# Performance work log

Measured on AMD Instinct MI355X. Metric: run time of the kernel, lower is better.

The kernel has to match this reference:

```python
import jax, jax.numpy as jnp
import numpy as np

B, LP, LR = 16, 128, 1024
D = 128
DG = 640  # 5 * 128 concat
K = 7     # number of FC trans heads
EDGE_P = 0.05


def _gcn_block(x, adj, mask, W1, b1, W2, b2):
    # x: [B,L,DG], adj: [B,L,L] (nonzero => edge weight 1, like dense_to_sparse + GCNConv)
    A = (adj != 0).astype(x.dtype)
    L = A.shape[-1]
    eye = jnp.eye(L, dtype=x.dtype)
    Ah = jnp.maximum(A, eye)                     # add_remaining_self_loops
    deg = Ah.sum(axis=1)                         # col degree [B,L] (gcn_norm uses target index)
    dinv = jax.lax.rsqrt(deg)                    # deg >= 1 thanks to self loops
    N = Ah * dinv[:, :, None] * dinv[:, None, :] # normalized adjacency per edge (r,c)
    agg = lambda h: jnp.einsum('brc,brd->bcd', N, h)  # aggregate sources r into target c
    h1 = jax.nn.relu(agg(x @ W1) + b1)
    h2 = agg(h1 @ W2) + b2
    return jax.nn.relu(x + h2) * mask[..., None]


def _fc_trans(feature, Wt, bt):
    # feature: [B,L,DG]; Wt: [K,D,DG]; bt: [K,D]
    h = jnp.einsum('bld,kod->kblo', feature, Wt) + bt[:, None, None, :]
    h = jax.nn.relu(h)                 # FCNet [640->128], ReLU (dropout off in eval)
    return jnp.swapaxes(h, 2, 3)       # [K,B,D,L] (transpose(1,2))


def _forward(x_pep, x_ss_pep, x_2_pep, x_dense_pep, x_pretrain_pep,
             x_pro, x_ss_pro, x_2_pro, x_dense_pro, x_pretrain_pro,
             x_edge_pep, x_edge_pro, x_seqmask_pep, x_seqmask_pro,
             E_seq, E_ss, E_two, W_dpep, b_dpep, W_dpro, b_dpro,
             W_ppep, b_ppep, W_ppro, b_ppro,
             Wg_pep1, bg_pep1, Wg_pep2, bg_pep2,
             Wg_pro1, bg_pro1, Wg_pro2, bg_pro2,
             Wt_pep, bt_pep, Wt_pro, bt_pro):
    enc_pep = jnp.concatenate([
        E_seq[x_pep], E_ss[x_ss_pep], E_two[x_2_pep],
        x_dense_pep @ W_dpep + b_dpep,
        x_pretrain_pep @ W_ppep + b_ppep], axis=-1) * x_seqmask_pep[..., None]
    enc_pro = jnp.concatenate([
        E_seq[x_pro], E_ss[x_ss_pro], E_two[x_2_pro],
        x_dense_pro @ W_dpro + b_dpro,
        x_pretrain_pro @ W_ppro + b_ppro], axis=-1) * x_seqmask_pro[..., None]

    f_pep = _gcn_block(enc_pep, x_edge_pep, x_seqmask_pep, Wg_pep1, bg_pep1, Wg_pep2, bg_pep2)
    f_pro = _gcn_block(enc_pro, x_edge_pro, x_seqmask_pro, Wg_pro1, bg_pro1, Wg_pro2, bg_pro2)

    pep_vecs = _fc_trans(f_pep, Wt_pep, bt_pep)[..., None]        # [K,B,D,LP,1] (unsqueeze 3)
    pro_vecs = _fc_trans(f_pro, Wt_pro, bt_pro)[:, :, :, None, :]  # [K,B,D,1,LR] (unsqueeze 2)
    return pep_vecs, pro_vecs


def setup_inputs() -> dict:
    key = jax.random.key(0)
    ks = jax.random.split(key, 40)
    f32 = jnp.float32
    s = 0.05
    inp = {
        'x_pep': jax.random.randint(ks[0], (B, LP), 0, 25),
        'x_ss_pep': jax.random.randint(ks[1], (B, LP), 0, 73),
        'x_2_pep': jax.random.randint(ks[2], (B, LP), 0, 8),
        'x_dense_pep': jax.random.normal(ks[3], (B, LP, 3), f32),
        'x_pretrain_pep': jax.random.normal(ks[4], (B, LP, 1024), f32),
        'x_pro': jax.random.randint(ks[5], (B, LR), 0, 25),
        'x_ss_pro': jax.random.randint(ks[6], (B, LR), 0, 73),
        'x_2_pro': jax.random.randint(ks[7], (B, LR), 0, 8),
        'x_dense_pro': jax.random.normal(ks[8], (B, LR, 23), f32),
        'x_pretrain_pro': jax.random.normal(ks[9], (B, LR, 1024), f32),
        'x_edge_pep': (jax.random.uniform(ks[10], (B, LP, LP)) < EDGE_P).astype(f32),
        'x_edge_pro': (jax.random.uniform(ks[11], (B, LR, LR)) < EDGE_P).astype(f32),
        'x_seqmask_pep': jnp.ones((B, LP), f32),
        'x_seqmask_pro': jnp.ones((B, LR), f32),
        'E_seq': jax.random.normal(ks[12], (25, D), f32) * s,
        'E_ss': jax.random.normal(ks[13], (73, D), f32) * s,
        'E_two': jax.random.normal(ks[14], (8, D), f32) * s,
        'W_dpep': jax.random.normal(ks[15], (3, D), f32) * s,
        'b_dpep': jnp.zeros((D,), f32),
        'W_dpro': jax.random.normal(ks[16], (23, D), f32) * s,
        'b_dpro': jnp.zeros((D,), f32),
        'W_ppep': jax.random.normal(ks[17], (1024, D), f32) * s,
        'b_ppep': jnp.zeros((D,), f32),
        'W_ppro': jax.random.normal(ks[18], (1024, D), f32) * s,
        'b_ppro': jnp.zeros((D,), f32),
        'Wg_pep1': jax.random.normal(ks[19], (DG, DG), f32) * s,
        'bg_pep1': jnp.zeros((DG,), f32),
        'Wg_pep2': jax.random.normal(ks[20], (DG, DG), f32) * s,
        'bg_pep2': jnp.zeros((DG,), f32),
        'Wg_pro1': jax.random.normal(ks[21], (DG, DG), f32) * s,
        'bg_pro1': jnp.zeros((DG,), f32),
        'Wg_pro2': jax.random.normal(ks[22], (DG, DG), f32) * s,
        'bg_pro2': jnp.zeros((DG,), f32),
        'Wt_pep': jax.random.normal(ks[23], (K, D, DG), f32) * s,
        'bt_pep': jnp.zeros((K, D), f32),
        'Wt_pro': jax.random.normal(ks[24], (K, D, DG), f32) * s,
        'bt_pro': jnp.zeros((K, D), f32),
    }
    return inp


def reference(x_pep, x_ss_pep, x_2_pep, x_dense_pep, x_pretrain_pep,
              x_pro, x_ss_pro, x_2_pro, x_dense_pro, x_pretrain_pro,
              x_edge_pep, x_edge_pro, x_seqmask_pep, x_seqmask_pro,
              E_seq, E_ss, E_two, W_dpep, b_dpep, W_dpro, b_dpro,
              W_ppep, b_ppep, W_ppro, b_ppro,
              Wg_pep1, bg_pep1, Wg_pep2, bg_pep2,
              Wg_pro1, bg_pro1, Wg_pro2, bg_pro2,
              Wt_pep, bt_pep, Wt_pro, bt_pro):
    return _forward(x_pep, x_ss_pep, x_2_pep, x_dense_pep, x_pretrain_pep,
                    x_pro, x_ss_pro, x_2_pro, x_dense_pro, x_pretrain_pro,
                    x_edge_pep, x_edge_pro, x_seqmask_pep, x_seqmask_pro,
                    E_seq, E_ss, E_two, W_dpep, b_dpep, W_dpro, b_dpro,
                    W_ppep, b_ppep, W_ppro, b_ppro,
                    Wg_pep1, bg_pep1, Wg_pep2, bg_pep2,
                    Wg_pro1, bg_pro1, Wg_pro2, bg_pro2,
                    Wt_pep, bt_pep, Wt_pro, bt_pro)
```

## Files before the change

### kernel.cpp

```cpp
#include <hip/hip_runtime.h>
#include <hip/hip_bf16.h>

#define BSZ 16
#define LP 128
#define LR 1024
#define DD 128
#define DG 640
#define KH 7
#define SPLITK 4

typedef __bf16 bf16x8 __attribute__((ext_vector_type(8)));
typedef __bf16 bf16x4v __attribute__((ext_vector_type(4)));
typedef float f32x4 __attribute__((ext_vector_type(4)));
typedef unsigned int uint32;

__device__ __forceinline__ void gl16(const void* g, void* l) {
  __builtin_amdgcn_global_load_lds(
      (const __attribute__((address_space(1))) unsigned int*)g,
      (__attribute__((address_space(3))) unsigned int*)l, 16, 0, 0);
}

__device__ __forceinline__ void mfma_core_lds(
    const ushort* __restrict__ Ab, int lda,
    const ushort* __restrict__ Bb, int ldb,
    int m0, int n0, int kStart, int kEnd, f32x4 (&acc)[4][4]) {
  __shared__ __align__(16) ushort As[128 * 64];
  __shared__ __align__(16) ushort Bs[128 * 64];
  int t = threadIdx.x;
  int wave = t >> 6, lane = t & 63;
  int quad = lane >> 4, l16 = lane & 15;
  int wm = (wave >> 1) * 64, wn = (wave & 1) * 64;

  int row0 = (wave * 256 + lane) >> 3;
  int s0 = lane & 7;
  const ushort* aBase = Ab + (size_t)(m0 + row0) * lda + s0 * 8;
  const ushort* bBase = Bb + (size_t)(n0 + row0) * ldb + s0 * 8;

  for (int k0 = kStart; k0 < kEnd; k0 += 64) {
    #pragma unroll
    for (int i = 0; i < 4; ++i) {
      gl16(aBase + (size_t)i * 8 * lda + k0, &As[wave * 2048 + i * 512]);
      gl16(bBase + (size_t)i * 8 * ldb + k0, &Bs[wave * 2048 + i * 512]);
    }
    __syncthreads();
    #pragma unroll
    for (int kc = 0; kc < 2; ++kc) {
      bf16x8 af[4], bfr[4];
      #pragma unroll
      for (int fi = 0; fi < 4; ++fi)
        af[fi] = *(const bf16x8*)&As[(wm + fi * 16 + l16) * 64 + kc * 32 + quad * 8];
      #pragma unroll
      for (int fj = 0; fj < 4; ++fj)
        bfr[fj] = *(const bf16x8*)&Bs[(wn + fj * 16 + l16) * 64 + kc * 32 + quad * 8];
      #pragma unroll
      for (int fi = 0; fi < 4; ++fi)
        #pragma unroll
        for (int fj = 0; fj < 4; ++fj)
          acc[fi][fj] = __builtin_amdgcn_mfma_f32_16x16x32_bf16(
              af[fi], bfr[fj], acc[fi][fj], 0, 0, 0);
    }
    __syncthreads();
  }
}

__device__ __forceinline__ void mfma_core_f32(
    const float* __restrict__ Af, int lda,
    const ushort* __restrict__ Bb, int ldb,
    int m0, int n0, int kStart, int kEnd, f32x4 (&acc)[4][4]) {
  __shared__ __align__(16) ushort As[128 * 72];
  __shared__ __align__(16) ushort Bs[128 * 72];
  int t = threadIdx.x;
  int wave = t >> 6, lane = t & 63;
  int quad = lane >> 4, l16 = lane & 15;
  int wm = (wave >> 1) * 64, wn = (wave & 1) * 64;
  int r1 = t >> 2, o1 = (t & 3) * 16;

  int4 b00, b01, b10, b11;
  float4 af32[8];

  auto load_k = [&](int k0) {
    b00 = *(const int4*)(Bb + (size_t)(n0 + r1) * ldb + k0 + o1);
    b01 = *(const int4*)(Bb + (size_t)(n0 + r1) * ldb + k0 + o1 + 8);
    b10 = *(const int4*)(Bb + (size_t)(n0 + r1 + 64) * ldb + k0 + o1);
    b11 = *(const int4*)(Bb + (size_t)(n0 + r1 + 64) * ldb + k0 + o1 + 8);
    #pragma unroll
    for (int s = 0; s < 8; ++s) {
      int idx = t + s * 256;
      int row = idx >> 4, c4 = (idx & 15) * 4;
      af32[s] = *(const float4*)(Af + (size_t)(m0 + row) * lda + k0 + c4);
    }
  };

  load_k(kStart);
  for (int k0 = kStart; k0 < kEnd; k0 += 64) {
    __syncthreads();
    #pragma unroll
    for (int s = 0; s < 8; ++s) {
      int idx = t + s * 256;
      int row = idx >> 4, c4 = (idx & 15) * 4;
      ushort4 u; __bf16 h;
      h = (__bf16)af32[s].x; u.x = *(ushort*)&h;
      h = (__bf16)af32[s].y; u.y = *(ushort*)&h;
      h = (__bf16)af32[s].z; u.z = *(ushort*)&h;
      h = (__bf16)af32[s].w; u.w = *(ushort*)&h;
      *(ushort4*)&As[row * 72 + c4] = u;
    }
    *(int4*)&Bs[r1 * 72 + o1] = b00;
    *(int4*)&Bs[r1 * 72 + o1 + 8] = b01;
    *(int4*)&Bs[(r1 + 64) * 72 + o1] = b10;
    *(int4*)&Bs[(r1 + 64) * 72 + o1 + 8] = b11;
    __syncthreads();
    if (k0 + 64 < kEnd) load_k(k0 + 64);
    #pragma unroll
    for (int kc = 0; kc < 2; ++kc) {
      bf16x8 af[4], bfr[4];
      #pragma unroll
      for (int fi = 0; fi < 4; ++fi)
        af[fi] = *(const bf16x8*)&As[(wm + fi * 16 + l16) * 72 + kc * 32 + quad * 8];
      #pragma unroll
      for (int fj = 0; fj < 4; ++fj)
        bfr[fj] = *(const bf16x8*)&Bs[(wn + fj * 16 + l16) * 72 + kc * 32 + quad * 8];
      #pragma unroll
      for (int fi = 0; fi < 4; ++fi)
        #pragma unroll
        for (int fj = 0; fj < 4; ++fj)
          acc[fi][fj] = __builtin_amdgcn_mfma_f32_16x16x32_bf16(
              af[fi], bfr[fj], acc[fi][fj], 0, 0, 0);
    }
  }
}

__device__ __forceinline__ void agg_core(
    const uint32* __restrict__ pb, int L,
    const ushort* __restrict__ Bb, int ldb,
    int m0, int n0, f32x4 (&acc)[4][4]) {
  __shared__ __align__(16) ushort Bs[128 * 64];
  __shared__ uint32 Aw[2][128];
  int t = threadIdx.x;
  int wave = t >> 6, lane = t & 63;
  int quad = lane >> 4, l16 = lane & 15;
  int wm = (wave >> 1) * 64, wn = (wave & 1) * 64;
  int half = t >> 7, cc = t & 127;

  int row0 = (wave * 256 + lane) >> 3;
  int s0 = lane & 7;
  const ushort* bBase = Bb + (size_t)(n0 + row0) * ldb + s0 * 8;
  const uint32* pbBase = pb + (size_t)half * L + m0 + cc;

  for (int k0 = 0; k0 < L; k0 += 64) {
    #pragma unroll
    for (int i = 0; i < 4; ++i)
      gl16(bBase + (size_t)i * 8 * ldb + k0, &Bs[wave * 2048 + i * 512]);
    Aw[half][cc] = pbBase[(size_t)(k0 >> 5) * L];
    __syncthreads();
    #pragma unroll
    for (int kc = 0; kc < 2; ++kc) {
      bf16x8 af[4], bfr[4];
      #pragma unroll
      for (int fj = 0; fj < 4; ++fj)
        bfr[fj] = *(const bf16x8*)&Bs[(wn + fj * 16 + l16) * 64 + kc * 32 + quad * 8];
      #pragma unroll
      for (int fi = 0; fi < 4; ++fi) {
        uint32 bits = (Aw[kc][wm + fi * 16 + l16] >> (quad * 8)) & 0xffu;
        int4 p;
        p.x = (int)((((bits >> 0) & 1) ? 0x3F80u : 0u) | (((bits >> 1) & 1) ? 0x3F800000u : 0u));
        p.y = (int)((((bits >> 2) & 1) ? 0x3F80u : 0u) | (((bits >> 3) & 1) ? 0x3F800000u : 0u));
        p.z = (int)((((bits >> 4) & 1) ? 0x3F80u : 0u) | (((bits >> 5) & 1) ? 0x3F800000u : 0u));
        p.w = (int)((((bits >> 6) & 1) ? 0x3F80u : 0u) | (((bits >> 7) & 1) ? 0x3F800000u : 0u));
        af[fi] = *(bf16x8*)&p;
      }
      #pragma unroll
      for (int fi = 0; fi < 4; ++fi)
        #pragma unroll
        for (int fj = 0; fj < 4; ++fj)
          acc[fi][fj] = __builtin_amdgcn_mfma_f32_16x16x32_bf16(
              af[fi], bfr[fj], acc[fi][fj], 0, 0, 0);
    }
    __syncthreads();
  }
}

__device__ __forceinline__ void tr_tile(const float* __restrict__ src,
                                        __bf16* __restrict__ dst,
                                        int R, int C, int cb, int rb, int t) {
  __shared__ float T[32][33];
  int r0 = rb * 32, c0 = cb * 32;
  #pragma unroll
  for (int s = 0; s < 4; ++s) {
    int idx = t + s * 256;
    int r = idx >> 5, c = idx & 31;
    T[r][c] = src[(size_t)(r0 + r) * C + c0 + c];
  }
  __syncthreads();
  #pragma unroll
  for (int s = 0; s < 4; ++s) {
    int idx = t + s * 256;
    int c = idx >> 5, r = idx & 31;
    dst[(size_t)(c0 + c) * R + r0 + r] = (__bf16)T[r][c];
  }
}

__global__ __launch_bounds__(256) void prep_weights(
    const float* __restrict__ Wppep, const float* __restrict__ Wppro,
    const float* __restrict__ Wg1p, const float* __restrict__ Wg2p,
    const float* __restrict__ Wg1r, const float* __restrict__ Wg2r,
    const float* __restrict__ Wtp, const float* __restrict__ Wtr,
    __bf16* __restrict__ WppTp, __bf16* __restrict__ WppTr,
    __bf16* __restrict__ Wg1Tp, __bf16* __restrict__ Wg2Tp,
    __bf16* __restrict__ Wg1Tr, __bf16* __restrict__ Wg2Tr,
    __bf16* __restrict__ WtBp, __bf16* __restrict__ WtBr) {
  int z = blockIdx.z, bx = blockIdx.x, t = threadIdx.x;
  if (z < 2) {
    if (bx >= 128) return;
    tr_tile(z ? Wppro : Wppep, z ? WppTr : WppTp, 1024, 128, bx % 4, bx / 4, t);
  } else if (z < 6) {
    if (bx >= 400) return;
    const float* src = (z == 2) ? Wg1p : (z == 3) ? Wg2p : (z == 4) ? Wg1r : Wg2r;
    __bf16* dst = (z == 2) ? Wg1Tp : (z == 3) ? Wg2Tp : (z == 4) ? Wg1Tr : Wg2Tr;
    tr_tile(src, dst, 640, 640, bx % 20, bx / 20, t);
  } else {
    if (bx >= 560) return;
    const float* src = (z == 6) ? Wtp : Wtr;
    __bf16* dst = (z == 6) ? WtBp : WtBr;
    int i = bx * 256 + t;
    float4 v = ((const float4*)src)[i];
    bf16x4v o;
    o.x = (__bf16)v.x; o.y = (__bf16)v.y; o.z = (__bf16)v.z; o.w = (__bf16)v.w;
    ((bf16x4v*)dst)[i] = o;
  }
}

__global__ __launch_bounds__(256) void zero_f32(float* __restrict__ p, int n) {
  int i = blockIdx.x * 256 + threadIdx.x;
  if (i < n) p[i] = 0.f;
}

__global__ __launch_bounds__(256) void rsqrt_k(const float* __restrict__ deg,
                                               float* __restrict__ dinv, int n) {
  int i = blockIdx.x * 256 + threadIdx.x;
  if (i < n) dinv[i] = rsqrtf(deg[i]);
}

__global__ __launch_bounds__(256) void prep_pack_merged(
    const float* __restrict__ adjP, const float* __restrict__ adjR,
    uint32* __restrict__ packedP, uint32* __restrict__ packedR,
    float* __restrict__ degP, float* __restrict__ degR) {
  int t = threadIdx.x;
  const float* adj; uint32* packed; float* deg;
  int b, rw, c, L;
  if (blockIdx.z < 16) {
    L = LR; b = blockIdx.z; rw = blockIdx.y; c = blockIdx.x * 256 + t;
    adj = adjR; packed = packedR; deg = degR;
  } else {
    L = LP; b = blockIdx.y; rw = blockIdx.x; c = t;
    if (b >= 16 || c >= LP) return;
    adj = adjP; packed = packedP; deg = degP;
  }
  const float* adjB = adj + (size_t)b * L * L;
  uint32 w = 0;
  int rbase = rw * 32;
  #pragma unroll 8
  for (int j = 0; j < 32; ++j) {
    float a = adjB[(size_t)(rbase + j) * L + c];
    if (a != 0.f || (rbase + j) == c) w |= (1u << j);
  }
  packed[((size_t)b * (L >> 5) + rw) * L + c] = w;
  atomicAdd(deg + b * L + c, (float)__popc(w));
}

__global__ __launch_bounds__(256) void pre_gemm(
    const float* __restrict__ XpP, const float* __restrict__ XpR,
    const __bf16* __restrict__ WppTp, const __bf16* __restrict__ WppTr,
    float* __restrict__ partP, float* __restrict__ partR) {
  int bx = blockIdx.x, s = blockIdx.y;
  int pep = bx < (BSZ * LP / 128);
  int m0 = (pep ? bx : bx - BSZ * LP / 128) * 128;
  const float* A = pep ? XpP : XpR;
  const ushort* B = (const ushort*)(pep ? WppTp : WppTr);
  int BL = pep ? BSZ * LP : BSZ * LR;
  float* part = (pep ? partP : partR) + (size_t)s * BL * DD;

  f32x4 acc[4][4];
  #pragma unroll
  for (int i = 0; i < 4; ++i)
    #pragma unroll
    for (int j = 0; j < 4; ++j) acc[i][j] = (f32x4){0.f, 0.f, 0.f, 0.f};
  mfma_core_f32(A, 1024, B, 1024, m0, 0, s * (1024 / SPLITK),
                (s + 1) * (1024 / SPLITK), acc);

  int t = threadIdx.x;
  int wave = t >> 6, lane = t & 63;
  int quad = lane >> 4, l16 = lane & 15;
  int wm = (wave >> 1) * 64, wn = (wave & 1) * 64;
  #pragma unroll
  for (int fi = 0; fi < 4; ++fi)
    #pragma unroll
    for (int r = 0; r < 4; ++r) {
      int m = m0 + wm + fi * 16 + quad * 4 + r;
      #pragma unroll
      for (int fj = 0; fj < 4; ++fj) {
        int n = wn + fj * 16 + l16;
        part[(size_t)m * DD + n] = acc[fi][fj][r];
      }
    }
}

__global__ __launch_bounds__(128) void encoder_merged(
    const int* __restrict__ xsP, const int* __restrict__ xssP,
    const int* __restrict__ x2P, const float* __restrict__ xdP,
    const float* __restrict__ WdP, const float* __restrict__ bdP,
    const float* __restrict__ maskP, const float* __restrict__ partP,
    const float* __restrict__ bppP, __bf16* __restrict__ encP,
    const int* __restrict__ xsR, const int* __restrict__ xssR,
    const int* __restrict__ x2R, const float* __restrict__ xdR,
    const float* __restrict__ WdR, const float* __restrict__ bdR,
    const float* __restrict__ maskR, const float* __restrict__ partR,
    const float* __restrict__ bppR, __bf16* __restrict__ encR,
    const float* __restrict__ Eseq, const float* __restrict__ Ess,
    const float* __restrict__ Etwo) {
  int gw = blockIdx.x;
  int t = threadIdx.x;
  int pep = gw < BSZ * LP;
  int row = pep ? gw : gw - BSZ * LP;
  int BL = pep ? BSZ * LP : BSZ * LR;
  int Kd = pep ? 3 : 23;
  const int* xs = pep ? xsP : xsR;
  const int* xss = pep ? xssP : xssR;
  const int* x2 = pep ? x2P : x2R;
  const float* xd = pep ? xdP : xdR;
  const float* Wd = pep ? WdP : WdR;
  const float* bd = pep ? bdP : bdR;
  const float* mask = pep ? maskP : maskR;
  const float* part = pep ? partP : partR;
  const float* bpp = pep ? bppP : bppR;
  __bf16* enc = pep ? encP : encR;

  float m = mask[row];
  int i0 = xs[row], i1 = xss[row], i2 = x2[row];
  __bf16* e = enc + (size_t)row * DG;
  e[t]        = (__bf16)(Eseq[i0 * DD + t] * m);
  e[DD + t]   = (__bf16)(Ess[i1 * DD + t] * m);
  e[2*DD + t] = (__bf16)(Etwo[i2 * DD + t] * m);
  float acc = bd[t];
  const float* xr = xd + (size_t)row * Kd;
  for (int i = 0; i < Kd; ++i) acc = fmaf(xr[i], Wd[i * DD + t], acc);
  e[3*DD + t] = (__bf16)(acc * m);
  float p = bpp[t];
  #pragma unroll
  for (int s = 0; s < SPLITK; ++s)
    p += part[(size_t)s * BL * DD + (size_t)row * DD + t];
  e[4*DD + t] = (__bf16)(p * m);
}

__global__ __launch_bounds__(256) void linT_merged(
    const __bf16* __restrict__ WgTp, const __bf16* __restrict__ srcP,
    const float* __restrict__ dinvP, __bf16* __restrict__ dstP,
    const __bf16* __restrict__ WgTr, const __bf16* __restrict__ srcR,
    const float* __restrict__ dinvR, __bf16* __restrict__ dstR) {
  int bx = blockIdx.x;
  int pep = bx < (BSZ * LP / 128);
  int n0 = (pep ? bx : bx - BSZ * LP / 128) * 128;
  int m0 = blockIdx.y * 128;
  int BL = pep ? BSZ * LP : BSZ * LR;
  const ushort* A = (const ushort*)(pep ? WgTp : WgTr);
  const ushort* B = (const ushort*)(pep ? srcP : srcR);
  const float* dinv = pep ? dinvP : dinvR;
  __bf16* dst = pep ? dstP : dstR;

  f32x4 acc[4][4];
  #pragma unroll
  for (int i = 0; i < 4; ++i)
    #pragma unroll
    for (int j = 0; j < 4; ++j) acc[i][j] = (f32x4){0.f, 0.f, 0.f, 0.f};
  mfma_core_lds(A, DG, B, DG, m0, n0, 0, DG, acc);

  int t = threadIdx.x;
  int wave = t >> 6, lane = t & 63;
  int quad = lane >> 4, l16 = lane & 15;
  int wm = (wave >> 1) * 64, wn = (wave & 1) * 64;
  #pragma unroll
  for (int fi = 0; fi < 4; ++fi)
    #pragma unroll
    for (int r = 0; r < 4; ++r) {
      int m = m0 + wm + fi * 16 + quad * 4 + r;
      #pragma unroll
      for (int fj = 0; fj < 4; ++fj) {
        int n = n0 + wn + fj * 16 + l16;
        dst[(size_t)m * BL + n] = (__bf16)(acc[fi][fj][r] * dinv[n]);
      }
    }
}

__global__ __launch_bounds__(256) void agg_merged(
    const uint32* __restrict__ packedP, const __bf16* __restrict__ XtP,
    const float* __restrict__ dinvP, const float* __restrict__ biasP,
    const __bf16* __restrict__ encEP, const float* __restrict__ maskP,
    __bf16* __restrict__ YP,
    const uint32* __restrict__ packedR, const __bf16* __restrict__ XtR,
    const float* __restrict__ dinvR, const float* __restrict__ biasR,
    const __bf16* __restrict__ encER, const float* __restrict__ maskR,
    __bf16* __restrict__ YR) {
  int bx = blockIdx.x;
  int b = bx / 5;
  int n0 = (bx % 5) * 128;
  int pep = (blockIdx.y == 0);
  int L = pep ? LP : LR;
  int BL = BSZ * L;
  int m0 = pep ? 0 : (blockIdx.y - 1) * 128;
  const uint32* pb = (pep ? packedP : packedR) + (size_t)b * (L >> 5) * L;
  const ushort* Bb = (const ushort*)(pep ? XtP : XtR) + (size_t)b * L;
  const float* dinv = pep ? dinvP : dinvR;
  const float* bias = pep ? biasP : biasR;
  const __bf16* encE = pep ? encEP : encER;
  const float* mask = pep ? maskP : maskR;
  __bf16* Y = pep ? YP : YR;

  f32x4 acc[4][4];
  #pragma unroll
  for (int i = 0; i < 4; ++i)
    #pragma unroll
    for (int j = 0; j < 4; ++j) acc[i][j] = (f32x4){0.f, 0.f, 0.f, 0.f};
  agg_core(pb, L, Bb, BL, m0, n0, acc);

  int t = threadIdx.x;
  int wave = t >> 6, lane = t & 63;
  int quad = lane >> 4, l16 = lane & 15;
  int wm = (wave >> 1) * 64, wn = (wave & 1) * 64;
  int gRow = b * L;
  #pragma unroll
  for (int fi = 0; fi < 4; ++fi)
    #pragma unroll
    for (int r = 0; r < 4; ++r) {
      int m = m0 + wm + fi * 16 + quad * 4 + r;
      int gi = gRow + m;
      float di = dinv[gi];
      float rm = mask ? mask[gi] : 1.f;
      #pragma unroll
      for (int fj = 0; fj < 4; ++fj) {
        int n = n0 + wn + fj * 16 + l16;
        float v = acc[fi][fj][r] * di + bias[n];
        if (encE) v += (float)encE[(size_t)gi * DG + n];
        v = fmaxf(v, 0.f);
        v *= rm;
        Y[(size_t)gi * DG + n] = (__bf16)v;
      }
    }
}

__global__ __launch_bounds__(256) void fct_merged(
    const __bf16* __restrict__ WtBp, const float* __restrict__ btp,
    const __bf16* __restrict__ Yp, float* __restrict__ outP,
    const __bf16* __restrict__ WtBr, const float* __restrict__ btr,
    const __bf16* __restrict__ Yr, float* __restrict__ outR) {
  int kh = blockIdx.y;
  int pro = (blockIdx.z < 16);
  const ushort* A;
  const ushort* B;
  const float* bt;
  int n0;
  if (pro) {
    A = (const ushort*)(WtBr + (size_t)kh * DD * DG);
    B = (const ushort*)(Yr + (size_t)blockIdx.z * LR * DG);
    bt = btr;
    n0 = blockIdx.x * 128;
  } else {
    A = (const ushort*)(WtBp + (size_t)kh * DD * DG);
    B = (const ushort*)Yp;
    bt = btp;
    n0 = ((blockIdx.z - 16) * 8 + blockIdx.x) * 128;
  }

  f32x4 acc[4][4];
  #pragma unroll
  for (int i = 0; i < 4; ++i)
    #pragma unroll
    for (int j = 0; j < 4; ++j) acc[i][j] = (f32x4){0.f, 0.f, 0.f, 0.f};
  mfma_core_lds(A, DG, B, DG, 0, n0, 0, DG, acc);

  int t = threadIdx.x;
  int wave = t >> 6, lane = t & 63;
  int quad = lane >> 4, l16 = lane & 15;
  int wm = (wave >> 1) * 64, wn = (wave & 1) * 64;
  #pragma unroll
  for (int fi = 0; fi < 4; ++fi)
    #pragma unroll
    for (int r = 0; r < 4; ++r) {
      int m = wm + fi * 16 + quad * 4 + r;
      float bb = bt[kh * DD + m];
      #pragma unroll
      for (int fj = 0; fj < 4; ++fj) {
        int n = n0 + wn + fj * 16 + l16;
        float v = fmaxf(acc[fi][fj][r] + bb, 0.f);
        if (pro) {
          outR[((size_t)(kh * BSZ + blockIdx.z) * DD + m) * LR + n] = v;
        } else {
          int b = n >> 7, l = n & 127;
          outP[((size_t)(kh * BSZ + b) * DD + m) * LP + l] = v;
        }
      }
    }
}

extern "C" void kernel_launch(void* const* d_in, const int* in_sizes, int n_in,
                              void* d_out, int out_size, void* d_ws, size_t ws_size,
                              hipStream_t stream) {
  const int*   x_pep          = (const int*)d_in[0];
  const int*   x_ss_pep       = (const int*)d_in[1];
  const int*   x_2_pep        = (const int*)d_in[2];
  const float* x_dense_pep    = (const float*)d_in[3];
  const float* x_pretrain_pep = (const float*)d_in[4];
  const int*   x_pro          = (const int*)d_in[5];
  const int*   x_ss_pro       = (const int*)d_in[6];
  const int*   x_2_pro        = (const int*)d_in[7];
  const float* x_dense_pro    = (const float*)d_in[8];
  const float* x_pretrain_pro = (const float*)d_in[9];
  const float* x_edge_pep     = (const float*)d_in[10];
  const float* x_edge_pro     = (const float*)d_in[11];
  const float* mask_pep       = (const float*)d_in[12];
  const float* mask_pro       = (const float*)d_in[13];
  const float* E_seq          = (const float*)d_in[14];
  const float* E_ss           = (const float*)d_in[15];
  const float* E_two          = (const float*)d_in[16];
  const float* W_dpep         = (const float*)d_in[17];
  const float* b_dpep         = (const float*)d_in[18];
  const float* W_dpro         = (const float*)d_in[19];
  const float* b_dpro         = (const float*)d_in[20];
  const float* W_ppep         = (const float*)d_in[21];
  const float* b_ppep         = (const float*)d_in[22];
  const float* W_ppro         = (const float*)d_in[23];
  const float* b_ppro         = (const float*)d_in[24];
  const float* Wg_pep1        = (const float*)d_in[25];
  const float* bg_pep1        = (const float*)d_in[26];
  const float* Wg_pep2        = (const float*)d_in[27];
  const float* bg_pep2        = (const float*)d_in[28];
  const float* Wg_pro1        = (const float*)d_in[29];
  const float* bg_pro1        = (const float*)d_in[30];
  const float* Wg_pro2        = (const float*)d_in[31];
  const float* bg_pro2        = (const float*)d_in[32];
  const float* Wt_pep         = (const float*)d_in[33];
  const float* bt_pep         = (const float*)d_in[34];
  const float* Wt_pro         = (const float*)d_in[35];
  const float* bt_pro         = (const float*)d_in[36];

  float* out = (float*)d_out;
  const int BLp = BSZ * LP;
  const int BLr = BSZ * LR;
  const size_t out_pro_off = (size_t)KH * BSZ * DD * LP;

  char* w = (char*)d_ws;
  __bf16* encBp  = (__bf16*)w; w += (size_t)BLp * DG * 2;
  __bf16* encBr  = (__bf16*)w; w += (size_t)BLr * DG * 2;
  __bf16* bufATp = (__bf16*)w; w += (size_t)DG * BLp * 2;
  __bf16* bufATr = (__bf16*)w; w += (size_t)DG * BLr * 2;
  __bf16* bufYp  = (__bf16*)w; w += (size_t)BLp * DG * 2;
  __bf16* bufYr  = (__bf16*)w; w += (size_t)BLr * DG * 2;
  __bf16* WppTp  = (__bf16*)w; w += (size_t)DD * 1024 * 2;
  __bf16* WppTr  = (__bf16*)w; w += (size_t)DD * 1024 * 2;
  __bf16* Wg1Tp  = (__bf16*)w; w += (size_t)DG * DG * 2;
  __bf16* Wg2Tp  = (__bf16*)w; w += (size_t)DG * DG * 2;
  __bf16* Wg1Tr  = (__bf16*)w; w += (size_t)DG * DG * 2;
  __bf16* Wg2Tr  = (__bf16*)w; w += (size_t)DG * DG * 2;
  __bf16* WtBp   = (__bf16*)w; w += (size_t)KH * DD * DG * 2;
  __bf16* WtBr   = (__bf16*)w; w += (size_t)KH * DD * DG * 2;
  uint32* packedP = (uint32*)w; w += (size_t)BSZ * (LP / 32) * LP * 4;
  uint32* packedR = (uint32*)w; w += (size_t)BSZ * (LR / 32) * LR * 4;
  float* degP  = (float*)w; w += (size_t)BLp * 4;
  float* degR  = (float*)w; w += (size_t)BLr * 4;
  float* dinvP = (float*)w; w += (size_t)BLp * 4;
  float* dinvR = (float*)w; w += (size_t)BLr * 4;
  float* partP = (float*)w; w += (size_t)SPLITK * BLp * DD * 4;
  float* partR = (float*)w; w += (size_t)SPLITK * BLr * DD * 4;

  prep_weights<<<dim3(560, 1, 8), 256, 0, stream>>>(
      W_ppep, W_ppro, Wg_pep1, Wg_pep2, Wg_pro1, Wg_pro2, Wt_pep, Wt_pro,
      WppTp, WppTr, Wg1Tp, Wg2Tp, Wg1Tr, Wg2Tr, WtBp, WtBr);
  zero_f32<<<(BLp + BLr) / 256, 256, 0, stream>>>(degP, BLp + BLr);
  prep_pack_merged<<<dim3(4, 32, 17), 256, 0, stream>>>(
      x_edge_pep, x_edge_pro, packedP, packedR, degP, degR);
  rsqrt_k<<<(BLp + BLr) / 256, 256, 0, stream>>>(degP, dinvP, BLp + BLr);
  pre_gemm<<<dim3((BLp + BLr) / 128, SPLITK), 256, 0, stream>>>(
      x_pretrain_pep, x_pretrain_pro, WppTp, WppTr, partP, partR);
  encoder_merged<<<BLp + BLr, 128, 0, stream>>>(
      x_pep, x_ss_pep, x_2_pep, x_dense_pep, W_dpep, b_dpep, mask_pep, partP,
      b_ppep, encBp,
      x_pro, x_ss_pro, x_2_pro, x_dense_pro, W_dpro, b_dpro, mask_pro, partR,
      b_ppro, encBr,
      E_seq, E_ss, E_two);
  linT_merged<<<dim3((BLp + BLr) / 128, DG / 128), 256, 0, stream>>>(
      Wg1Tp, encBp, dinvP, bufATp, Wg1Tr, encBr, dinvR, bufATr);
  agg_merged<<<dim3(80, 9), 256, 0, stream>>>(
      packedP, bufATp, dinvP, bg_pep1, nullptr, nullptr, bufYp,
      packedR, bufATr, dinvR, bg_pro1, nullptr, nullptr, bufYr);
  linT_merged<<<dim3((BLp + BLr) / 128, DG / 128), 256, 0, stream>>>(
      Wg2Tp, bufYp, dinvP, bufATp, Wg2Tr, bufYr, dinvR, bufATr);
  agg_merged<<<dim3(80, 9), 256, 0, stream>>>(
      packedP, bufATp, dinvP, bg_pep2, encBp, mask_pep, bufYp,
      packedR, bufATr, dinvR, bg_pro2, encBr, mask_pro, bufYr);
  fct_merged<<<dim3(LR / 128, KH, 18), 256, 0, stream>>>(
      WtBp, bt_pep, bufYp, out,
      WtBr, bt_pro, bufYr, out + out_pro_off);
}
```

Baseline: 495.8 us.

## Expand adjacency to dense bf16 and double-buffer the LDS MFMA GEMM core

Adds an expand_adj kernel that unpacks the bit-packed adjacency into a dense transposed bf16 matrix, stored in the reused split-K partial buffer. Aggregation then runs through the generic LDS GEMM core, which drops the per-iteration bit-to-bf16 decoding in agg_core. That core is rewritten to use 32-wide K tiles with double buffering, XOR-swizzled LDS slots and one barrier per step, so global loads overlap MFMA work. The cost is writing and reading a 32 MB dense adjacency instead of a 1-bit packed form, plus one extra kernel launch.

```diff
diff --git a/kernel.cpp b/kernel.cpp
--- a/kernel.cpp
+++ b/kernel.cpp
@@ -24,42 +24,54 @@
     const ushort* __restrict__ Ab, int lda,
     const ushort* __restrict__ Bb, int ldb,
     int m0, int n0, int kStart, int kEnd, f32x4 (&acc)[4][4]) {
-  __shared__ __align__(16) ushort As[128 * 64];
-  __shared__ __align__(16) ushort Bs[128 * 64];
+  __shared__ __align__(16) ushort As[2][128 * 32];
+  __shared__ __align__(16) ushort Bs[2][128 * 32];
   int t = threadIdx.x;
   int wave = t >> 6, lane = t & 63;
   int quad = lane >> 4, l16 = lane & 15;
   int wm = (wave >> 1) * 64, wn = (wave & 1) * 64;
 
-  int row0 = (wave * 256 + lane) >> 3;
-  int s0 = lane & 7;
-  const ushort* aBase = Ab + (size_t)(m0 + row0) * lda + s0 * 8;
-  const ushort* bBase = Bb + (size_t)(n0 + row0) * ldb + s0 * 8;
-
-  for (int k0 = kStart; k0 < kEnd; k0 += 64) {
-    #pragma unroll
-    for (int i = 0; i < 4; ++i) {
-      gl16(aBase + (size_t)i * 8 * lda + k0, &As[wave * 2048 + i * 512]);
-      gl16(bBase + (size_t)i * 8 * ldb + k0, &Bs[wave * 2048 + i * 512]);
-    }
-    __syncthreads();
-    #pragma unroll
-    for (int kc = 0; kc < 2; ++kc) {
-      bf16x8 af[4], bfr[4];
-      #pragma unroll
-      for (int fi = 0; fi < 4; ++fi)
-        af[fi] = *(const bf16x8*)&As[(wm + fi * 16 + l16) * 64 + kc * 32 + quad * 8];
+  int rowBase = wave * 32 + (lane >> 2);
+  int cg = (lane & 3) ^ ((lane >> 3) & 3);
+  const ushort* aSrc = Ab + (size_t)(m0 + rowBase) * lda + cg * 8 + kStart;
+  const ushort* bSrc = Bb + (size_t)(n0 + rowBase) * ldb + cg * 8 + kStart;
+  int ldsW = wave * 1024;
+
+  auto issue = [&](int buf, int kOff) {
+    #pragma unroll
+    for (int i = 0; i < 2; ++i) {
+      gl16(aSrc + (size_t)i * 16 * lda + kOff, &As[buf][ldsW + i * 512]);
+      gl16(bSrc + (size_t)i * 16 * ldb + kOff, &Bs[buf][ldsW + i * 512]);
+    }
+  };
+
+  int nIter = (kEnd - kStart) >> 5;
+  issue(0, 0);
+  asm volatile("s_waitcnt vmcnt(0)" ::: "memory");
+  __builtin_amdgcn_s_barrier();
+
+  int slot = (quad ^ ((l16 >> 1) & 3)) * 8;
+  int buf = 0;
+  for (int it = 0; it < nIter; ++it) {
+    if (it + 1 < nIter) issue(buf ^ 1, (it + 1) * 32);
+    bf16x8 af[4], bfr[4];
+    #pragma unroll
+    for (int fi = 0; fi < 4; ++fi)
+      af[fi] = *(const bf16x8*)&As[buf][(wm + fi * 16 + l16) * 32 + slot];
+    #pragma unroll
+    for (int fj = 0; fj < 4; ++fj)
+      bfr[fj] = *(const bf16x8*)&Bs[buf][(wn + fj * 16 + l16) * 32 + slot];
+    #pragma unroll
+    for (int fi = 0; fi < 4; ++fi)
       #pragma unroll
       for (int fj = 0; fj < 4; ++fj)
-        bfr[fj] = *(const bf16x8*)&Bs[(wn + fj * 16 + l16) * 64 + kc * 32 + quad * 8];
-      #pragma unroll
-      for (int fi = 0; fi < 4; ++fi)
-        #pragma unroll
-        for (int fj = 0; fj < 4; ++fj)
-          acc[fi][fj] = __builtin_amdgcn_mfma_f32_16x16x32_bf16(
-              af[fi], bfr[fj], acc[fi][fj], 0, 0, 0);
-    }
-    __syncthreads();
+        acc[fi][fj] = __builtin_amdgcn_mfma_f32_16x16x32_bf16(
+            af[fi], bfr[fj], acc[fi][fj], 0, 0, 0);
+    if (it + 1 < nIter) {
+      asm volatile("s_waitcnt vmcnt(0)" ::: "memory");
+      __builtin_amdgcn_s_barrier();
+      buf ^= 1;
+    }
   }
 }
 
@@ -127,56 +139,6 @@
           acc[fi][fj] = __builtin_amdgcn_mfma_f32_16x16x32_bf16(
               af[fi], bfr[fj], acc[fi][fj], 0, 0, 0);
     }
-  }
-}
-
-__device__ __forceinline__ void agg_core(
-    const uint32* __restrict__ pb, int L,
-    const ushort* __restrict__ Bb, int ldb,
-    int m0, int n0, f32x4 (&acc)[4][4]) {
-  __shared__ __align__(16) ushort Bs[128 * 64];
-  __shared__ uint32 Aw[2][128];
-  int t = threadIdx.x;
-  int wave = t >> 6, lane = t & 63;
-  int quad = lane >> 4, l16 = lane & 15;
-  int wm = (wave >> 1) * 64, wn = (wave & 1) * 64;
-  int half = t >> 7, cc = t & 127;
-
-  int row0 = (wave * 256 + lane) >> 3;
-  int s0 = lane & 7;
-  const ushort* bBase = Bb + (size_t)(n0 + row0) * ldb + s0 * 8;
-  const uint32* pbBase = pb + (size_t)half * L + m0 + cc;
-
-  for (int k0 = 0; k0 < L; k0 += 64) {
-    #pragma unroll
-    for (int i = 0; i < 4; ++i)
-      gl16(bBase + (size_t)i * 8 * ldb + k0, &Bs[wave * 2048 + i * 512]);
-    Aw[half][cc] = pbBase[(size_t)(k0 >> 5) * L];
-    __syncthreads();
-    #pragma unroll
-    for (int kc = 0; kc < 2; ++kc) {
-      bf16x8 af[4], bfr[4];
-      #pragma unroll
-      for (int fj = 0; fj < 4; ++fj)
-        bfr[fj] = *(const bf16x8*)&Bs[(wn + fj * 16 + l16) * 64 + kc * 32 + quad * 8];
-      #pragma unroll
-      for (int fi = 0; fi < 4; ++fi) {
-        uint32 bits = (Aw[kc][wm + fi * 16 + l16] >> (quad * 8)) & 0xffu;
-        int4 p;
-        p.x = (int)((((bits >> 0) & 1) ? 0x3F80u : 0u) | (((bits >> 1) & 1) ? 0x3F800000u : 0u));
-        p.y = (int)((((bits >> 2) & 1) ? 0x3F80u : 0u) | (((bits >> 3) & 1) ? 0x3F800000u : 0u));
-        p.z = (int)((((bits >> 4) & 1) ? 0x3F80u : 0u) | (((bits >> 5) & 1) ? 0x3F800000u : 0u));
-        p.w = (int)((((bits >> 6) & 1) ? 0x3F80u : 0u) | (((bits >> 7) & 1) ? 0x3F800000u : 0u));
-        af[fi] = *(bf16x8*)&p;
-      }
-      #pragma unroll
-      for (int fi = 0; fi < 4; ++fi)
-        #pragma unroll
-        for (int fj = 0; fj < 4; ++fj)
-          acc[fi][fj] = __builtin_amdgcn_mfma_f32_16x16x32_bf16(
-              af[fi], bfr[fj], acc[fi][fj], 0, 0, 0);
-    }
-    __syncthreads();
   }
 }
 
@@ -268,6 +230,32 @@
   atomicAdd(deg + b * L + c, (float)__popc(w));
 }
 
+__global__ __launch_bounds__(256) void expand_adj(
+    const uint32* __restrict__ packedP, const uint32* __restrict__ packedR,
+    __bf16* __restrict__ AhTp, __bf16* __restrict__ AhTr) {
+  int bx = blockIdx.x, t = threadIdx.x;
+  uint32 wbits;
+  __bf16* drow;
+  if (bx < 2048) {
+    int b = bx >> 7, c = (bx & 127) * 8 + (t >> 5), rw = t & 31;
+    wbits = packedR[((size_t)b * 32 + rw) * LR + c];
+    drow = AhTr + ((size_t)b * LR + c) * LR + rw * 32;
+  } else {
+    int bb = bx - 2048;
+    int b = bb >> 1, c = (bb & 1) * 64 + (t >> 2), rw = t & 3;
+    wbits = packedP[((size_t)b * 4 + rw) * LP + c];
+    drow = AhTp + ((size_t)b * LP + c) * LP + rw * 32;
+  }
+  int4 o[4];
+  uint32* op = (uint32*)o;
+  #pragma unroll
+  for (int p = 0; p < 16; ++p)
+    op[p] = (((wbits >> (2 * p)) & 1u) ? 0x3F80u : 0u) |
+            (((wbits >> (2 * p + 1)) & 1u) ? 0x3F800000u : 0u);
+  int4* d4 = (int4*)drow;
+  d4[0] = o[0]; d4[1] = o[1]; d4[2] = o[2]; d4[3] = o[3];
+}
+
 __global__ __launch_bounds__(256) void pre_gemm(
     const float* __restrict__ XpP, const float* __restrict__ XpR,
     const __bf16* __restrict__ WppTp, const __bf16* __restrict__ WppTr,
@@ -392,11 +380,11 @@
 }
 
 __global__ __launch_bounds__(256) void agg_merged(
-    const uint32* __restrict__ packedP, const __bf16* __restrict__ XtP,
+    const __bf16* __restrict__ AhTp, const __bf16* __restrict__ XtP,
     const float* __restrict__ dinvP, const float* __restrict__ biasP,
     const __bf16* __restrict__ encEP, const float* __restrict__ maskP,
     __bf16* __restrict__ YP,
-    const uint32* __restrict__ packedR, const __bf16* __restrict__ XtR,
+    const __bf16* __restrict__ AhTr, const __bf16* __restrict__ XtR,
     const float* __restrict__ dinvR, const float* __restrict__ biasR,
     const __bf16* __restrict__ encER, const float* __restrict__ maskR,
     __bf16* __restrict__ YR) {
@@ -407,7 +395,7 @@
   int L = pep ? LP : LR;
   int BL = BSZ * L;
   int m0 = pep ? 0 : (blockIdx.y - 1) * 128;
-  const uint32* pb = (pep ? packedP : packedR) + (size_t)b * (L >> 5) * L;
+  const ushort* Ab = (const ushort*)(pep ? AhTp : AhTr) + (size_t)b * L * L;
   const ushort* Bb = (const ushort*)(pep ? XtP : XtR) + (size_t)b * L;
   const float* dinv = pep ? dinvP : dinvR;
   const float* bias = pep ? biasP : biasR;
@@ -420,7 +408,7 @@
   for (int i = 0; i < 4; ++i)
     #pragma unroll
     for (int j = 0; j < 4; ++j) acc[i][j] = (f32x4){0.f, 0.f, 0.f, 0.f};
-  agg_core(pb, L, Bb, BL, m0, n0, acc);
+  mfma_core_lds(Ab, L, Bb, BL, m0, n0, 0, L, acc);
 
   int t = threadIdx.x;
   int wave = t >> 6, lane = t & 63;
@@ -571,6 +559,9 @@
   float* partP = (float*)w; w += (size_t)SPLITK * BLp * DD * 4;
   float* partR = (float*)w; w += (size_t)SPLITK * BLr * DD * 4;
 
+  __bf16* AhTp = (__bf16*)partP;
+  __bf16* AhTr = (__bf16*)partR;
+
   prep_weights<<<dim3(560, 1, 8), 256, 0, stream>>>(
       W_ppep, W_ppro, Wg_pep1, Wg_pep2, Wg_pro1, Wg_pro2, Wt_pep, Wt_pro,
       WppTp, WppTr, Wg1Tp, Wg2Tp, Wg1Tr, Wg2Tr, WtBp, WtBr);
@@ -586,16 +577,17 @@
       x_pro, x_ss_pro, x_2_pro, x_dense_pro, W_dpro, b_dpro, mask_pro, partR,
       b_ppro, encBr,
       E_seq, E_ss, E_two);
+  expand_adj<<<2080, 256, 0, stream>>>(packedP, packedR, AhTp, AhTr);
   linT_merged<<<dim3((BLp + BLr) / 128, DG / 128), 256, 0, stream>>>(
       Wg1Tp, encBp, dinvP, bufATp, Wg1Tr, encBr, dinvR, bufATr);
   agg_merged<<<dim3(80, 9), 256, 0, stream>>>(
-      packedP, bufATp, dinvP, bg_pep1, nullptr, nullptr, bufYp,
-      packedR, bufATr, dinvR, bg_pro1, nullptr, nullptr, bufYr);
+      AhTp, bufATp, dinvP, bg_pep1, nullptr, nullptr, bufYp,
+      AhTr, bufATr, dinvR, bg_pro1, nullptr, nullptr, bufYr);
   linT_merged<<<dim3((BLp + BLr) / 128, DG / 128), 256, 0, stream>>>(
       Wg2Tp, bufYp, dinvP, bufATp, Wg2Tr, bufYr, dinvR, bufATr);
   agg_merged<<<dim3(80, 9), 256, 0, stream>>>(
-      packedP, bufATp, dinvP, bg_pep2, encBp, mask_pep, bufYp,
-      packedR, bufATr, dinvR, bg_pro2, encBr, mask_pro, bufYr);
+      AhTp, bufATp, dinvP, bg_pep2, encBp, mask_pep, bufYp,
+      AhTr, bufATr, dinvR, bg_pro2, encBr, mask_pro, bufYr);
   fct_merged<<<dim3(LR / 128, KH, 18), 256, 0, stream>>>(
       WtBp, bt_pep, bufYp, out,
       WtBr, bt_pro, bufYr, out + out_pro_off);
```

After: 513.3 us. +3.5%, slower.

## Replace direct global-to-LDS loads with register-prefetched, padded LDS pipeline

Applied to the files above, without the earlier changes.

Swaps the global_load_lds direct copies in the bf16 GEMM core and the adjacency aggregation core for register-staged loads that prefetch two K-tiles ahead, then write them into padded LDS tiles with a row stride of 72. The aim is to overlap global memory latency with MFMA compute and to remove LDS bank conflicts in the fragment reads that the unpadded 64-wide layout caused. In exchange it uses more registers for the prefetch buffers, which may lower occupancy, and adds extra barriers per tile.

```diff
diff --git a/kernel.cpp b/kernel.cpp
--- a/kernel.cpp
+++ b/kernel.cpp
@@ -14,44 +14,50 @@
 typedef float f32x4 __attribute__((ext_vector_type(4)));
 typedef unsigned int uint32;
 
-__device__ __forceinline__ void gl16(const void* g, void* l) {
-  __builtin_amdgcn_global_load_lds(
-      (const __attribute__((address_space(1))) unsigned int*)g,
-      (__attribute__((address_space(3))) unsigned int*)l, 16, 0, 0);
-}
-
-__device__ __forceinline__ void mfma_core_lds(
+__device__ __forceinline__ void mfma_core_bf16(
     const ushort* __restrict__ Ab, int lda,
     const ushort* __restrict__ Bb, int ldb,
     int m0, int n0, int kStart, int kEnd, f32x4 (&acc)[4][4]) {
-  __shared__ __align__(16) ushort As[128 * 64];
-  __shared__ __align__(16) ushort Bs[128 * 64];
+  __shared__ __align__(16) ushort As[128 * 72];
+  __shared__ __align__(16) ushort Bs[128 * 72];
   int t = threadIdx.x;
   int wave = t >> 6, lane = t & 63;
   int quad = lane >> 4, l16 = lane & 15;
   int wm = (wave >> 1) * 64, wn = (wave & 1) * 64;
-
-  int row0 = (wave * 256 + lane) >> 3;
-  int s0 = lane & 7;
-  const ushort* aBase = Ab + (size_t)(m0 + row0) * lda + s0 * 8;
-  const ushort* bBase = Bb + (size_t)(n0 + row0) * ldb + s0 * 8;
-
-  for (int k0 = kStart; k0 < kEnd; k0 += 64) {
-    #pragma unroll
-    for (int i = 0; i < 4; ++i) {
-      gl16(aBase + (size_t)i * 8 * lda + k0, &As[wave * 2048 + i * 512]);
-      gl16(bBase + (size_t)i * 8 * ldb + k0, &Bs[wave * 2048 + i * 512]);
-    }
-    __syncthreads();
+  int r1 = t >> 2, o1 = (t & 3) * 16;
+
+  int4 a0[4], b0[4], a1[4], b1[4];
+
+  auto load_k = [&](int k0, int4 (&a)[4], int4 (&b)[4]) {
+    b[0] = *(const int4*)(Bb + (size_t)(n0 + r1) * ldb + k0 + o1);
+    b[1] = *(const int4*)(Bb + (size_t)(n0 + r1) * ldb + k0 + o1 + 8);
+    b[2] = *(const int4*)(Bb + (size_t)(n0 + r1 + 64) * ldb + k0 + o1);
+    b[3] = *(const int4*)(Bb + (size_t)(n0 + r1 + 64) * ldb + k0 + o1 + 8);
+    a[0] = *(const int4*)(Ab + (size_t)(m0 + r1) * lda + k0 + o1);
+    a[1] = *(const int4*)(Ab + (size_t)(m0 + r1) * lda + k0 + o1 + 8);
+    a[2] = *(const int4*)(Ab + (size_t)(m0 + r1 + 64) * lda + k0 + o1);
+    a[3] = *(const int4*)(Ab + (size_t)(m0 + r1 + 64) * lda + k0 + o1 + 8);
+  };
+  auto stage = [&](int4 (&a)[4], int4 (&b)[4]) {
+    *(int4*)&As[r1 * 72 + o1] = a[0];
+    *(int4*)&As[r1 * 72 + o1 + 8] = a[1];
+    *(int4*)&As[(r1 + 64) * 72 + o1] = a[2];
+    *(int4*)&As[(r1 + 64) * 72 + o1 + 8] = a[3];
+    *(int4*)&Bs[r1 * 72 + o1] = b[0];
+    *(int4*)&Bs[r1 * 72 + o1 + 8] = b[1];
+    *(int4*)&Bs[(r1 + 64) * 72 + o1] = b[2];
+    *(int4*)&Bs[(r1 + 64) * 72 + o1 + 8] = b[3];
+  };
+  auto compute = [&]() {
     #pragma unroll
     for (int kc = 0; kc < 2; ++kc) {
       bf16x8 af[4], bfr[4];
       #pragma unroll
       for (int fi = 0; fi < 4; ++fi)
-        af[fi] = *(const bf16x8*)&As[(wm + fi * 16 + l16) * 64 + kc * 32 + quad * 8];
+        af[fi] = *(const bf16x8*)&As[(wm + fi * 16 + l16) * 72 + kc * 32 + quad * 8];
       #pragma unroll
       for (int fj = 0; fj < 4; ++fj)
-        bfr[fj] = *(const bf16x8*)&Bs[(wn + fj * 16 + l16) * 64 + kc * 32 + quad * 8];
+        bfr[fj] = *(const bf16x8*)&Bs[(wn + fj * 16 + l16) * 72 + kc * 32 + quad * 8];
       #pragma unroll
       for (int fi = 0; fi < 4; ++fi)
         #pragma unroll
@@ -59,7 +65,24 @@
           acc[fi][fj] = __builtin_amdgcn_mfma_f32_16x16x32_bf16(
               af[fi], bfr[fj], acc[fi][fj], 0, 0, 0);
     }
+  };
+
+  int nIter = (kEnd - kStart) >> 6;
+  load_k(kStart, a0, b0);
+  if (nIter > 1) load_k(kStart + 64, a1, b1);
+  for (int it = 0; it < nIter; it += 2) {
     __syncthreads();
+    stage(a0, b0);
+    __syncthreads();
+    if (it + 2 < nIter) load_k(kStart + (it + 2) * 64, a0, b0);
+    compute();
+    if (it + 1 < nIter) {
+      __syncthreads();
+      stage(a1, b1);
+      __syncthreads();
+      if (it + 3 < nIter) load_k(kStart + (it + 3) * 64, a1, b1);
+      compute();
+    }
   }
 }
 
@@ -134,31 +157,39 @@
     const uint32* __restrict__ pb, int L,
     const ushort* __restrict__ Bb, int ldb,
     int m0, int n0, f32x4 (&acc)[4][4]) {
-  __shared__ __align__(16) ushort Bs[128 * 64];
+  __shared__ __align__(16) ushort Bs[128 * 72];
   __shared__ uint32 Aw[2][128];
   int t = threadIdx.x;
   int wave = t >> 6, lane = t & 63;
   int quad = lane >> 4, l16 = lane & 15;
   int wm = (wave >> 1) * 64, wn = (wave & 1) * 64;
+  int r1 = t >> 2, o1 = (t & 3) * 16;
   int half = t >> 7, cc = t & 127;
 
-  int row0 = (wave * 256 + lane) >> 3;
-  int s0 = lane & 7;
-  const ushort* bBase = Bb + (size_t)(n0 + row0) * ldb + s0 * 8;
-  const uint32* pbBase = pb + (size_t)half * L + m0 + cc;
-
-  for (int k0 = 0; k0 < L; k0 += 64) {
-    #pragma unroll
-    for (int i = 0; i < 4; ++i)
-      gl16(bBase + (size_t)i * 8 * ldb + k0, &Bs[wave * 2048 + i * 512]);
-    Aw[half][cc] = pbBase[(size_t)(k0 >> 5) * L];
-    __syncthreads();
+  int4 b0[4], b1[4];
+  uint32 w0, w1;
+
+  auto load_k = [&](int k0, int4 (&b)[4], uint32& w) {
+    b[0] = *(const int4*)(Bb + (size_t)(n0 + r1) * ldb + k0 + o1);
+    b[1] = *(const int4*)(Bb + (size_t)(n0 + r1) * ldb + k0 + o1 + 8);
+    b[2] = *(const int4*)(Bb + (size_t)(n0 + r1 + 64) * ldb + k0 + o1);
+    b[3] = *(const int4*)(Bb + (size_t)(n0 + r1 + 64) * ldb + k0 + o1 + 8);
+    w = pb[(size_t)((k0 >> 5) + half) * L + m0 + cc];
+  };
+  auto stage = [&](int4 (&b)[4], uint32 w) {
+    *(int4*)&Bs[r1 * 72 + o1] = b[0];
+    *(int4*)&Bs[r1 * 72 + o1 + 8] = b[1];
+    *(int4*)&Bs[(r1 + 64) * 72 + o1] = b[2];
+    *(int4*)&Bs[(r1 + 64) * 72 + o1 + 8] = b[3];
+    Aw[half][cc] = w;
+  };
+  auto compute = [&]() {
     #pragma unroll
     for (int kc = 0; kc < 2; ++kc) {
       bf16x8 af[4], bfr[4];
       #pragma unroll
       for (int fj = 0; fj < 4; ++fj)
-        bfr[fj] = *(const bf16x8*)&Bs[(wn + fj * 16 + l16) * 64 + kc * 32 + quad * 8];
+        bfr[fj] = *(const bf16x8*)&Bs[(wn + fj * 16 + l16) * 72 + kc * 32 + quad * 8];
       #pragma unroll
       for (int fi = 0; fi < 4; ++fi) {
         uint32 bits = (Aw[kc][wm + fi * 16 + l16] >> (quad * 8)) & 0xffu;
@@ -176,7 +207,24 @@
           acc[fi][fj] = __builtin_amdgcn_mfma_f32_16x16x32_bf16(
               af[fi], bfr[fj], acc[fi][fj], 0, 0, 0);
     }
+  };
+
+  int nIter = L >> 6;
+  load_k(0, b0, w0);
+  if (nIter > 1) load_k(64, b1, w1);
+  for (int it = 0; it < nIter; it += 2) {
     __syncthreads();
+    stage(b0, w0);
+    __syncthreads();
+    if (it + 2 < nIter) load_k((it + 2) * 64, b0, w0);
+    compute();
+    if (it + 1 < nIter) {
+      __syncthreads();
+      stage(b1, w1);
+      __syncthreads();
+      if (it + 3 < nIter) load_k((it + 3) * 64, b1, w1);
+      compute();
+    }
   }
 }
 
@@ -372,7 +420,7 @@
   for (int i = 0; i < 4; ++i)
     #pragma unroll
     for (int j = 0; j < 4; ++j) acc[i][j] = (f32x4){0.f, 0.f, 0.f, 0.f};
-  mfma_core_lds(A, DG, B, DG, m0, n0, 0, DG, acc);
+  mfma_core_bf16(A, DG, B, DG, m0, n0, 0, DG, acc);
 
   int t = threadIdx.x;
   int wave = t >> 6, lane = t & 63;
@@ -475,7 +523,7 @@
   for (int i = 0; i < 4; ++i)
     #pragma unroll
     for (int j = 0; j < 4; ++j) acc[i][j] = (f32x4){0.f, 0.f, 0.f, 0.f};
-  mfma_core_lds(A, DG, B, DG, 0, n0, 0, DG, acc);
+  mfma_core_bf16(A, DG, B, DG, 0, n0, 0, DG, acc);
 
   int t = threadIdx.x;
   int wave = t >> 6, lane = t & 63;
```

Result: slower. 756.1 us (+52.5%).
